# Optimization experiments

Hardware: AMD Instinct MI355X
Metric: run time of the kernel (lower is better)

Reference implementation:

```python
import jax, jax.numpy as jnp
import numpy as np

RES = 128
RES_V = RES + 1          # dense vertex grid resolution
N_VOX = 400000           # active sparse voxels
SDF_BIAS = -1.0 / RES
CUBE_CORNERS = jnp.array([[0,0,0],[1,0,0],[0,1,0],[1,1,0],
                          [0,0,1],[1,0,1],[0,1,1],[1,1,1]], dtype=jnp.int32)


def setup_inputs() -> dict:
    key = jax.random.key(0)
    k1, k2 = jax.random.split(key)
    coords = jax.random.randint(k1, (N_VOX, 3), 0, RES, dtype=jnp.int32)
    feats = jax.random.normal(k2, (N_VOX, 101), dtype=jnp.float32)
    return {"coords": coords, "feats": feats}


def reference(coords, feats):
    N = feats.shape[0]
    # layout: sdf[0:8] deform[8:32] weights[32:53] color[53:101]
    sdf = feats[:, 0:8].reshape(N, 8, 1) + SDF_BIAS
    deform = feats[:, 8:32].reshape(N, 8, 3)
    weights = feats[:, 32:53]                      # [N,21]
    color = feats[:, 53:101].reshape(N, 8, 6)
    value = jnp.concatenate([sdf, deform, color], axis=-1)   # [N,8,10]

    # cube-corner vertex ids on the dense (RES_V)^3 grid; identical to
    # torch.unique dedup + scatter_reduce(mean) + get_dense_attrs scatter.
    corner = coords[:, None, :] + CUBE_CORNERS[None]         # [N,8,3]
    vid = ((corner[..., 0] * RES_V + corner[..., 1]) * RES_V
           + corner[..., 2]).reshape(-1)                     # [N*8]
    n_verts = RES_V ** 3

    sums = jax.ops.segment_sum(value.reshape(-1, 10), vid, num_segments=n_verts)
    cnts = jax.ops.segment_sum(jnp.ones((N * 8,), feats.dtype), vid,
                               num_segments=n_verts)
    v_attrs = sums / jnp.maximum(cnts, 1.0)[:, None]         # mean, 0 if untouched

    sdf_d = v_attrs[:, 0]
    deform_d = v_attrs[:, 1:4]
    colors_d = v_attrs[:, 4:10]

    # regular dense vertex positions + tanh-bounded deformation
    vertsid = jnp.arange(n_verts)
    reg_v = jnp.stack([vertsid // (RES_V ** 2),
                       (vertsid // RES_V) % RES_V,
                       vertsid % RES_V], axis=1).astype(feats.dtype)
    x_nx3 = reg_v / RES - 0.5 + (1.0 - 1e-8) / (2.0 * RES) * jnp.tanh(deform_d)

    # dense flexicube weights grid (scatter-set at active voxels)
    cid = (coords[:, 0] * RES + coords[:, 1]) * RES + coords[:, 2]
    weights_d = jnp.zeros((RES ** 3, 21), feats.dtype).at[cid].set(weights)

    # [n_verts, 10]: deformed positions (3) | sdf (1) | colors+normals (6)
    v_out = jnp.concatenate([x_nx3, sdf_d[:, None], colors_d], axis=-1)
    return (v_out, weights_d)
```

## Files before the change

### kernel.cpp

```cpp
#include <hip/hip_runtime.h>

#define RES 128
#define RES_V 129
#define N_VOX 400000

constexpr int N_VERTS = RES_V * RES_V * RES_V;
constexpr int N_CELLS = RES * RES * RES;
constexpr long VOUT_WORDS = (long)N_VERTS * 10;
constexpr long OUTW_WORDS = (long)N_CELLS * 21;
constexpr int SCAN_BLOCKS = 512;
constexpr float SDF_BIAS = -1.0f / 128.0f;
constexpr float DEFORM_SCALE = (float)((1.0 - 1e-8) / 256.0);
constexpr float INV_RES = 1.0f / 128.0f;

static __device__ __forceinline__ unsigned int f2bf(float x) {
    unsigned int u = __float_as_uint(x);
    unsigned int r = ((u >> 16) & 1u) + 0x7FFFu;
    return (u + r) >> 16;
}
static __device__ __forceinline__ float bf_lo(unsigned int w) {
    return __uint_as_float(w << 16);
}
static __device__ __forceinline__ float bf_hi(unsigned int w) {
    return __uint_as_float(w & 0xFFFF0000u);
}

__global__ void __launch_bounds__(256) init_counts(unsigned int* __restrict__ counts)
{
    int t = blockIdx.x * blockDim.x + threadIdx.x;
    if (t < N_CELLS) counts[t] = 0u;
}

__global__ void __launch_bounds__(256) count_kernel(const int* __restrict__ coords,
                                                    unsigned int* __restrict__ counts)
{
    int n = blockIdx.x * blockDim.x + threadIdx.x;
    if (n >= N_VOX) return;
    int cx = coords[n * 3 + 0];
    int cy = coords[n * 3 + 1];
    int cz = coords[n * 3 + 2];
    int cid = (cx * RES + cy) * RES + cz;
    atomicAdd(counts + cid, 1u);
}

__global__ void __launch_bounds__(256) scan1_kernel(const unsigned int* __restrict__ counts,
                                                    unsigned int* __restrict__ starts,
                                                    unsigned int* __restrict__ blocksums)
{
    __shared__ unsigned int part[256];
    int b = blockIdx.x, t = threadIdx.x;
    long base = (long)b * 4096 + (long)t * 16;
    unsigned int v[16], s = 0;
#pragma unroll
    for (int i = 0; i < 16; ++i) { v[i] = counts[base + i]; s += v[i]; }
    part[t] = s;
    __syncthreads();
    for (int off = 1; off < 256; off <<= 1) {
        unsigned int x = (t >= off) ? part[t - off] : 0u;
        __syncthreads();
        part[t] += x;
        __syncthreads();
    }
    unsigned int excl = (t == 0) ? 0u : part[t - 1];
    if (t == 255) blocksums[b] = part[255];
    unsigned int run = excl;
#pragma unroll
    for (int i = 0; i < 16; ++i) { starts[base + i] = run; run += v[i]; }
}

__global__ void __launch_bounds__(512) scan2_kernel(unsigned int* __restrict__ blocksums)
{
    __shared__ unsigned int sh[SCAN_BLOCKS];
    int t = threadIdx.x;
    sh[t] = blocksums[t];
    __syncthreads();
    for (int off = 1; off < SCAN_BLOCKS; off <<= 1) {
        unsigned int x = (t >= off) ? sh[t - off] : 0u;
        __syncthreads();
        sh[t] += x;
        __syncthreads();
    }
    blocksums[t] = (t == 0) ? 0u : sh[t - 1];
}

__global__ void __launch_bounds__(256) fixup_kernel(unsigned int* __restrict__ starts,
                                                    unsigned int* __restrict__ cursors,
                                                    const unsigned int* __restrict__ blocksums)
{
    int t = blockIdx.x * blockDim.x + threadIdx.x;
    if (t >= N_CELLS) return;
    unsigned int g = starts[t] + blocksums[t >> 12];
    starts[t] = g;
    cursors[t] = g;
    if (t == 0) starts[N_CELLS] = (unsigned int)N_VOX;
}

__global__ void __launch_bounds__(256) fill_kernel(const int* __restrict__ coords,
                                                   unsigned int* __restrict__ cursors,
                                                   unsigned int* __restrict__ list)
{
    int n = blockIdx.x * blockDim.x + threadIdx.x;
    if (n >= N_VOX) return;
    int cx = coords[n * 3 + 0];
    int cy = coords[n * 3 + 1];
    int cz = coords[n * 3 + 2];
    int cid = (cx * RES + cy) * RES + cz;
    unsigned int slot = atomicAdd(cursors + cid, 1u);
    list[slot] = (unsigned int)n;
}

__global__ void __launch_bounds__(256) permute_kernel(const float* __restrict__ feats,
                                                      const unsigned int* __restrict__ list,
                                                      unsigned int* __restrict__ perm)
{
    int g = blockIdx.x * blockDim.x + threadIdx.x;
    int slot = g >> 3;
    int c = g & 7;
    if (slot >= N_VOX) return;
    long src = (long)list[slot] * 101;
    float v[10];
    v[0] = feats[src + c];
#pragma unroll
    for (int k = 0; k < 3; ++k) v[1 + k] = feats[src + 8 + 3 * c + k];
#pragma unroll
    for (int k = 0; k < 6; ++k) v[4 + k] = feats[src + 53 + 6 * c + k];
    unsigned int* d = perm + (long)slot * 40 + c * 5;
#pragma unroll
    for (int q = 0; q < 5; ++q)
        d[q] = f2bf(v[2 * q]) | (f2bf(v[2 * q + 1]) << 16);
}

__global__ void __launch_bounds__(256) gather_perm(const unsigned int* __restrict__ starts,
                                                   const unsigned int* __restrict__ perm,
                                                   float* __restrict__ vout)
{
    int vid = blockIdx.x * blockDim.x + threadIdx.x;
    if (vid >= N_VERTS) return;
    int z = vid % RES_V;
    int tmp = vid / RES_V;
    int y = tmp % RES_V;
    int x = tmp / RES_V;

    float sums[10];
#pragma unroll
    for (int j = 0; j < 10; ++j) sums[j] = 0.0f;
    int cnt = 0;

#pragma unroll
    for (int dx = 0; dx < 2; ++dx) {
        int cx = x - dx;
        if ((unsigned)cx >= RES) continue;
#pragma unroll
        for (int dy = 0; dy < 2; ++dy) {
            int cy = y - dy;
            if ((unsigned)cy >= RES) continue;
#pragma unroll
            for (int dz = 0; dz < 2; ++dz) {
                int cz = z - dz;
                if ((unsigned)cz >= RES) continue;
                int cid = (cx * RES + cy) * RES + cz;
                unsigned int s = starts[cid];
                unsigned int e = starts[cid + 1];
                if (s == e) continue;
                int c = dx + 2 * dy + 4 * dz;
                for (unsigned int i = s; i < e; ++i) {
                    const unsigned int* b = perm + (long)i * 40 + c * 5;
                    unsigned int w0 = b[0], w1 = b[1], w2 = b[2], w3 = b[3], w4 = b[4];
                    sums[0] += bf_lo(w0); sums[1] += bf_hi(w0);
                    sums[2] += bf_lo(w1); sums[3] += bf_hi(w1);
                    sums[4] += bf_lo(w2); sums[5] += bf_hi(w2);
                    sums[6] += bf_lo(w3); sums[7] += bf_hi(w3);
                    sums[8] += bf_lo(w4); sums[9] += bf_hi(w4);
                }
                cnt += (int)(e - s);
            }
        }
    }

    float fc = (float)cnt;
    float inv = 1.0f / fmaxf(fc, 1.0f);
    float o[10];
    o[0] = (float)x * INV_RES - 0.5f + DEFORM_SCALE * tanhf(sums[1] * inv);
    o[1] = (float)y * INV_RES - 0.5f + DEFORM_SCALE * tanhf(sums[2] * inv);
    o[2] = (float)z * INV_RES - 0.5f + DEFORM_SCALE * tanhf(sums[3] * inv);
    o[3] = (sums[0] + fc * SDF_BIAS) * inv;
#pragma unroll
    for (int j = 0; j < 6; ++j) o[4 + j] = sums[4 + j] * inv;

    float* p = vout + (long)vid * 10;
#pragma unroll
    for (int j = 0; j < 5; ++j)
        *(float2*)(p + 2 * j) = make_float2(o[2 * j], o[2 * j + 1]);
}

__global__ void __launch_bounds__(256) weights_fill2(const float* __restrict__ feats,
                                                     const unsigned int* __restrict__ starts,
                                                     const unsigned int* __restrict__ list,
                                                     float* __restrict__ outw)
{
    __shared__ float vals[256 * 21];
    int t = threadIdx.x;
    int cell0 = blockIdx.x * 256;
    int cell = cell0 + t;

    unsigned int s = starts[cell];
    unsigned int e = starts[cell + 1];
    if (e > s) {
        unsigned int li = 0u;
        for (unsigned int i = s; i < e; ++i) li = max(li, list[i]);
        const float* f = feats + (long)li * 101 + 32;
#pragma unroll
        for (int j = 0; j < 21; ++j) vals[t * 21 + j] = f[j];
    } else {
#pragma unroll
        for (int j = 0; j < 21; ++j) vals[t * 21 + j] = 0.0f;
    }
    __syncthreads();

    float* dst = outw + (long)cell0 * 21;
#pragma unroll
    for (int k = 0; k < 21; ++k) dst[t + 256 * k] = vals[t + 256 * k];
}

extern "C" void kernel_launch(void* const* d_in, const int* in_sizes, int n_in,
                              void* d_out, int out_size, void* d_ws, size_t ws_size,
                              hipStream_t stream) {
    const int* coords = (const int*)d_in[0];
    const float* feats = (const float*)d_in[1];
    float* out = (float*)d_out;
    float* vout = out;
    float* outw = out + VOUT_WORDS;

    unsigned int* starts = (unsigned int*)d_ws;
    unsigned int* list = starts + (N_CELLS + 1);
    unsigned int* blocksums = list + N_VOX;

    unsigned int* perm = (unsigned int*)outw;
    unsigned int* counts = (unsigned int*)(outw + (OUTW_WORDS - N_CELLS - 16));

    init_counts<<<(N_CELLS + 255) / 256, 256, 0, stream>>>(counts);
    count_kernel<<<(N_VOX + 255) / 256, 256, 0, stream>>>(coords, counts);
    scan1_kernel<<<SCAN_BLOCKS, 256, 0, stream>>>(counts, starts, blocksums);
    scan2_kernel<<<1, SCAN_BLOCKS, 0, stream>>>(blocksums);
    fixup_kernel<<<(N_CELLS + 255) / 256, 256, 0, stream>>>(starts, counts, blocksums);
    fill_kernel<<<(N_VOX + 255) / 256, 256, 0, stream>>>(coords, counts, list);
    permute_kernel<<<(N_VOX * 8 + 255) / 256, 256, 0, stream>>>(feats, list, perm);
    gather_perm<<<(N_VERTS + 255) / 256, 256, 0, stream>>>(starts, perm, vout);
    weights_fill2<<<N_CELLS / 256, 256, 0, stream>>>(feats, starts, list, outw);
}
```

Before: 221.1 us.

## Pack cell counts into start offsets, fold block-sum scan, remap gather blocks per XCD

Drops the single-block scan2 launch: each fixup block now reduces the preceding block sums itself. The per-cell start offset is packed together with an 8-bit count in one word, so gather and weights kernels usually read one word per cell instead of two. Gather workgroup ids are remapped so consecutive vertex ranges land on the same XCD for L2 locality. This relies on offsets fitting in 24 bits and adds redundant block-sum reduction work in every fixup block.

```diff
diff --git a/kernel.cpp b/kernel.cpp
--- a/kernel.cpp
+++ b/kernel.cpp
@@ -9,6 +9,7 @@
 constexpr long VOUT_WORDS = (long)N_VERTS * 10;
 constexpr long OUTW_WORDS = (long)N_CELLS * 21;
 constexpr int SCAN_BLOCKS = 512;
+constexpr int GATHER_BLOCKS = (N_VERTS + 255) / 256;
 constexpr float SDF_BIAS = -1.0f / 128.0f;
 constexpr float DEFORM_SCALE = (float)((1.0 - 1e-8) / 256.0);
 constexpr float INV_RES = 1.0f / 128.0f;
@@ -44,7 +45,7 @@
 }
 
 __global__ void __launch_bounds__(256) scan1_kernel(const unsigned int* __restrict__ counts,
-                                                    unsigned int* __restrict__ starts,
+                                                    unsigned int* __restrict__ packed,
                                                     unsigned int* __restrict__ blocksums)
 {
     __shared__ unsigned int part[256];
@@ -65,34 +66,32 @@
     if (t == 255) blocksums[b] = part[255];
     unsigned int run = excl;
 #pragma unroll
-    for (int i = 0; i < 16; ++i) { starts[base + i] = run; run += v[i]; }
-}
-
-__global__ void __launch_bounds__(512) scan2_kernel(unsigned int* __restrict__ blocksums)
-{
-    __shared__ unsigned int sh[SCAN_BLOCKS];
+    for (int i = 0; i < 16; ++i) { packed[base + i] = run; run += v[i]; }
+}
+
+__global__ void __launch_bounds__(256) fixup2_kernel(unsigned int* __restrict__ packed,
+                                                     unsigned int* __restrict__ cnt_cursor,
+                                                     const unsigned int* __restrict__ blocksums)
+{
+    __shared__ unsigned int red[256];
     int t = threadIdx.x;
-    sh[t] = blocksums[t];
+    int cell0 = blockIdx.x * 256;
+    int R = cell0 >> 12;
+    unsigned int part = 0;
+    for (int j = t; j < R; j += 256) part += blocksums[j];
+    red[t] = part;
     __syncthreads();
-    for (int off = 1; off < SCAN_BLOCKS; off <<= 1) {
-        unsigned int x = (t >= off) ? sh[t - off] : 0u;
+    for (int off = 128; off > 0; off >>= 1) {
+        if (t < off) red[t] += red[t + off];
         __syncthreads();
-        sh[t] += x;
-        __syncthreads();
-    }
-    blocksums[t] = (t == 0) ? 0u : sh[t - 1];
-}
-
-__global__ void __launch_bounds__(256) fixup_kernel(unsigned int* __restrict__ starts,
-                                                    unsigned int* __restrict__ cursors,
-                                                    const unsigned int* __restrict__ blocksums)
-{
-    int t = blockIdx.x * blockDim.x + threadIdx.x;
-    if (t >= N_CELLS) return;
-    unsigned int g = starts[t] + blocksums[t >> 12];
-    starts[t] = g;
-    cursors[t] = g;
-    if (t == 0) starts[N_CELLS] = (unsigned int)N_VOX;
+    }
+    unsigned int P = red[0];
+    int cell = cell0 + t;
+    unsigned int g = packed[cell] + P;
+    unsigned int cnt = cnt_cursor[cell];
+    packed[cell] = g | (min(cnt, 255u) << 24);
+    cnt_cursor[cell] = g;
+    if (cell == 0) packed[N_CELLS] = (unsigned int)N_VOX;
 }
 
 __global__ void __launch_bounds__(256) fill_kernel(const int* __restrict__ coords,
@@ -130,12 +129,18 @@
         d[q] = f2bf(v[2 * q]) | (f2bf(v[2 * q + 1]) << 16);
 }
 
-__global__ void __launch_bounds__(256) gather_perm(const unsigned int* __restrict__ starts,
+__global__ void __launch_bounds__(256) gather_perm(const unsigned int* __restrict__ packed,
                                                    const unsigned int* __restrict__ perm,
                                                    float* __restrict__ vout)
 {
-    int vid = blockIdx.x * blockDim.x + threadIdx.x;
+    const int nwg = GATHER_BLOCKS;
+    const int q = nwg / 8, r = nwg % 8;
+    int bid = blockIdx.x;
+    int xcd = bid % 8, i = bid / 8;
+    int wg = (xcd < r ? xcd * (q + 1) : r * (q + 1) + (xcd - r) * q) + i;
+    int vid = wg * 256 + threadIdx.x;
     if (vid >= N_VERTS) return;
+
     int z = vid % RES_V;
     int tmp = vid / RES_V;
     int y = tmp % RES_V;
@@ -159,12 +164,15 @@
                 int cz = z - dz;
                 if ((unsigned)cz >= RES) continue;
                 int cid = (cx * RES + cy) * RES + cz;
-                unsigned int s = starts[cid];
-                unsigned int e = starts[cid + 1];
-                if (s == e) continue;
+                unsigned int w = packed[cid];
+                unsigned int cc = w >> 24;
+                if (cc == 0u) continue;
+                unsigned int s = w & 0xFFFFFFu;
+                unsigned int e = (cc == 255u) ? (packed[cid + 1] & 0xFFFFFFu)
+                                              : s + cc;
                 int c = dx + 2 * dy + 4 * dz;
-                for (unsigned int i = s; i < e; ++i) {
-                    const unsigned int* b = perm + (long)i * 40 + c * 5;
+                for (unsigned int ii = s; ii < e; ++ii) {
+                    const unsigned int* b = perm + (long)ii * 40 + c * 5;
                     unsigned int w0 = b[0], w1 = b[1], w2 = b[2], w3 = b[3], w4 = b[4];
                     sums[0] += bf_lo(w0); sums[1] += bf_hi(w0);
                     sums[2] += bf_lo(w1); sums[3] += bf_hi(w1);
@@ -194,7 +202,7 @@
 }
 
 __global__ void __launch_bounds__(256) weights_fill2(const float* __restrict__ feats,
-                                                     const unsigned int* __restrict__ starts,
+                                                     const unsigned int* __restrict__ packed,
                                                      const unsigned int* __restrict__ list,
                                                      float* __restrict__ outw)
 {
@@ -203,9 +211,11 @@
     int cell0 = blockIdx.x * 256;
     int cell = cell0 + t;
 
-    unsigned int s = starts[cell];
-    unsigned int e = starts[cell + 1];
-    if (e > s) {
+    unsigned int w = packed[cell];
+    unsigned int cc = w >> 24;
+    if (cc > 0u) {
+        unsigned int s = w & 0xFFFFFFu;
+        unsigned int e = (cc == 255u) ? (packed[cell + 1] & 0xFFFFFFu) : s + cc;
         unsigned int li = 0u;
         for (unsigned int i = s; i < e; ++i) li = max(li, list[i]);
         const float* f = feats + (long)li * 101 + 32;
@@ -231,20 +241,19 @@
     float* vout = out;
     float* outw = out + VOUT_WORDS;
 
-    unsigned int* starts = (unsigned int*)d_ws;
-    unsigned int* list = starts + (N_CELLS + 1);
+    unsigned int* packed = (unsigned int*)d_ws;
+    unsigned int* list = packed + (N_CELLS + 1);
     unsigned int* blocksums = list + N_VOX;
 
     unsigned int* perm = (unsigned int*)outw;
-    unsigned int* counts = (unsigned int*)(outw + (OUTW_WORDS - N_CELLS - 16));
-
-    init_counts<<<(N_CELLS + 255) / 256, 256, 0, stream>>>(counts);
-    count_kernel<<<(N_VOX + 255) / 256, 256, 0, stream>>>(coords, counts);
-    scan1_kernel<<<SCAN_BLOCKS, 256, 0, stream>>>(counts, starts, blocksums);
-    scan2_kernel<<<1, SCAN_BLOCKS, 0, stream>>>(blocksums);
-    fixup_kernel<<<(N_CELLS + 255) / 256, 256, 0, stream>>>(starts, counts, blocksums);
-    fill_kernel<<<(N_VOX + 255) / 256, 256, 0, stream>>>(coords, counts, list);
+    unsigned int* cnt_cursor = (unsigned int*)(outw + (OUTW_WORDS - N_CELLS - 16));
+
+    init_counts<<<(N_CELLS + 255) / 256, 256, 0, stream>>>(cnt_cursor);
+    count_kernel<<<(N_VOX + 255) / 256, 256, 0, stream>>>(coords, cnt_cursor);
+    scan1_kernel<<<SCAN_BLOCKS, 256, 0, stream>>>(cnt_cursor, packed, blocksums);
+    fixup2_kernel<<<N_CELLS / 256, 256, 0, stream>>>(packed, cnt_cursor, blocksums);
+    fill_kernel<<<(N_VOX + 255) / 256, 256, 0, stream>>>(coords, cnt_cursor, list);
     permute_kernel<<<(N_VOX * 8 + 255) / 256, 256, 0, stream>>>(feats, list, perm);
-    gather_perm<<<(N_VERTS + 255) / 256, 256, 0, stream>>>(starts, perm, vout);
-    weights_fill2<<<N_CELLS / 256, 256, 0, stream>>>(feats, starts, list, outw);
-}
+    gather_perm<<<GATHER_BLOCKS, 256, 0, stream>>>(packed, perm, vout);
+    weights_fill2<<<N_CELLS / 256, 256, 0, stream>>>(feats, packed, list, outw);
+}
```

Measured after the change: 227.0 us. 2.7% more time.
